# Optimization experiments

Hardware: AMD Instinct MI355X
Metric: run time of the kernel (lower is better)

Reference implementation:

```python
import jax, jax.numpy as jnp
import numpy as np

B, GL, GF, N = 4, 4, 128, 1024
CS, CN, NA = 32, 16, 16
S, HS = 512, 512


def squash(s, axis):
    # mag_sq/(1+mag_sq) * s/mag == s * mag/(1+mag_sq)
    mag_sq = jnp.sum(s * s, axis=axis, keepdims=True)
    return s * (jnp.sqrt(mag_sq) / (1.0 + mag_sq))


def routing(u_hat, n_iter=3):
    # u_hat: [M, I, J, U]; dynamic routing, softmax over J, squash over J (as in source)
    M, I, J, U = u_hat.shape
    b = jnp.zeros((I, J), dtype=u_hat.dtype)
    v = None
    for _ in range(n_iter):
        c = jax.nn.softmax(b, axis=1)                       # [I, J]
        s = jnp.einsum('ij,miju->mju', c, u_hat)            # [M, J, U]
        v = squash(s, axis=1)                               # squash over J (torch dim=2)
        b = b + jnp.einsum('miju,mju->mij', u_hat, v).mean(axis=0)
    return v


def setup_inputs():
    key = jax.random.key(0)
    ks = jax.random.split(key, 7)
    sc = 0.1
    return {
        'graph_embed': jax.random.normal(ks[0], (B, GL, GF, N), jnp.float32),
        'hidden': jax.random.normal(ks[1], (B, S, HS), jnp.float32),
        'Wp': jax.random.normal(ks[2], (GL, CS, GL, GF), jnp.float32) * sc,  # per-unit conv kernels
        'bp': jax.random.normal(ks[3], (GL, CS), jnp.float32) * sc,
        'Wg': jax.random.normal(ks[4], (CS, CN, CS, GL), jnp.float32) * sc,  # graph caps [I,J,U,K]
        'Wa': jax.random.normal(ks[5], (CS + HS,), jnp.float32) * sc,        # attention_1 weight
        'Ws': jax.random.normal(ks[6], (CN, NA, CS, CS), jnp.float32) * sc,  # aspect caps [I,J,U,K]
    }


def _per_example(x, h, Wp, bp, Wg, Wa, Ws):
    # x: [GL, GF, N], h: [S, HS]
    gl, gf, n = x.shape
    # primary capsules: each unit's conv kernel covers all (GL,GF) -> full contraction
    u = jnp.einsum('uclf,lfn->ucn', Wp, x) + bp[:, :, None]   # [GL, CS, N]
    u = squash(u.reshape(gl, -1), axis=1)                     # squash over CS*N (torch dim=2)
    p = u.reshape(n, gl, CS)                                  # torch .view(-1, GL, CS)
    # graph capsule routing
    u_hat_g = jnp.einsum('ijuk,mik->miju', Wg, p.transpose(0, 2, 1))  # [N, CS, CN, CS]
    v_g = routing(u_hat_g)                                    # [N, CN, CS]
    g = v_g.reshape(n, CS, CN).mean(axis=0).reshape(CN, CS)   # torch .view semantics
    # adaptive attention: Linear([g;h]) with no bias, softmax over capsules
    score = jax.nn.softmax((g @ Wa[:CS])[None, :] + (h @ Wa[CS:])[:, None], axis=1)  # [S, CN]
    condensed = g[None, :, :] * score[:, :, None]             # [S, CN, CS]
    # aspect capsule routing (transpose(1,2) then layer-internal transpose cancel out)
    u_hat_a = jnp.einsum('ijuk,mik->miju', Ws, condensed)     # [S, CN, NA, CS]
    return routing(u_hat_a)                                   # [S, NA, CS]


def reference(graph_embed, hidden, Wp, bp, Wg, Wa, Ws):
    f = jax.vmap(_per_example, in_axes=(0, 0, None, None, None, None, None))
    return f(graph_embed, hidden, Wp, bp, Wg, Wa, Ws)   # [B, S, NA, CS]
```

## Files before the change

### kernel.cpp

```cpp
#include <hip/hip_runtime.h>
#include <math.h>


static constexpr int OFF_U   = 0;
static constexpr int OFF_S   = 524288;
static constexpr int OFF_SSP = 2621440;
static constexpr int OFF_BGP = 2621696;
static constexpr int OFF_GP  = 2654464;
static constexpr int OFF_VA  = 2687232;
static constexpr int OFF_MS  = 2689280;
static constexpr int OFF_UH  = 2820352;
static constexpr int OFF_WGR = 2853120;

__global__ void k_primaryF(const float* __restrict__ X, const float* __restrict__ Wp,
                           const float* __restrict__ bp,
                           float* __restrict__ U, float* __restrict__ SSp,
                           const float* __restrict__ Wg, float* __restrict__ Wgr)
{
    __shared__ float Wt[128 * 68];
    __shared__ float red[256];
    const int t = threadIdx.x;
    if (blockIdx.z == 4) {
        const int blk = blockIdx.x * 16 + blockIdx.y;
#pragma unroll
        for (int r = 0; r < 8; ++r) {
            const int e = blk * 2048 + r * 256 + t;
            const int q = e >> 9, rem = e & 511;
            const int u = rem >> 4, j = rem & 15;
            const int i = q & 31, kk = q >> 5;
            Wgr[e] = Wg[((i * 16 + j) * 32 + u) * 4 + kk];
        }
        return;
    }
    const int ct = blockIdx.x, nt = blockIdx.y, b = blockIdx.z;
    const int tn = t & 15, tc = t >> 4;
    const int c0 = ct * 64, n0 = nt * 64;
    float acc[4][4] = {};
    for (int ks = 0; ks < 4; ++ks) {
        if (ks) __syncthreads();
#pragma unroll
        for (int i = 0; i < 8; ++i) {
            const int idx = t + i * 256;
            const int c = idx >> 5, k4 = idx & 31;
            const float4 wv = *(const float4*)&Wp[(size_t)(c0 + c) * 512 + ks * 128 + k4 * 4];
            Wt[(k4 * 4 + 0) * 68 + c] = wv.x;
            Wt[(k4 * 4 + 1) * 68 + c] = wv.y;
            Wt[(k4 * 4 + 2) * 68 + c] = wv.z;
            Wt[(k4 * 4 + 3) * 68 + c] = wv.w;
        }
        __syncthreads();
        const float* Xp = X + (size_t)b * 524288 + (size_t)(ks * 128) * 1024 + n0 + tn * 4;
#pragma unroll 4
        for (int k = 0; k < 128; ++k) {
            const float4 xv = *(const float4*)(Xp + (size_t)k * 1024);
            const float4 wv = *(const float4*)&Wt[k * 68 + tc * 4];
            const float w[4] = {wv.x, wv.y, wv.z, wv.w};
            const float x[4] = {xv.x, xv.y, xv.z, xv.w};
#pragma unroll
            for (int ci = 0; ci < 4; ++ci)
#pragma unroll
                for (int ni = 0; ni < 4; ++ni)
                    acc[ci][ni] = fmaf(w[ci], x[ni], acc[ci][ni]);
        }
    }
    float ssq = 0.f;
#pragma unroll
    for (int ci = 0; ci < 4; ++ci) {
        const int c = c0 + tc * 4 + ci;
        const float bv = bp[c];
        float4 o = make_float4(acc[ci][0] + bv, acc[ci][1] + bv,
                               acc[ci][2] + bv, acc[ci][3] + bv);
        ssq = fmaf(o.x, o.x, ssq); ssq = fmaf(o.y, o.y, ssq);
        ssq = fmaf(o.z, o.z, ssq); ssq = fmaf(o.w, o.w, ssq);
        *(float4*)&U[(size_t)b * 131072 + (size_t)c * 1024 + n0 + tn * 4] = o;
    }
    red[t] = ssq;
    __syncthreads();
    for (int s = 64; s > 0; s >>= 1) {
        if ((t & 127) < s) red[t] += red[t + s];
        __syncthreads();
    }
    if ((t & 127) == 0)
        SSp[(b * 4 + ct * 2 + (t >> 7)) * 16 + nt] = red[t];
}

__global__ __launch_bounds__(256) void k_smatmulM2(
    const float* __restrict__ U, const float* __restrict__ SSp,
    const float* __restrict__ Bgp, const float* __restrict__ Wgr,
    float* __restrict__ S, float* __restrict__ MS, float* __restrict__ Gp,
    const int bg0)
{
    __shared__ __align__(16) float Pt[64 * 68];
    __shared__ __align__(16) float Ct[64 * 160];
    __shared__ float cls[512];
    __shared__ float bgs[512];
    __shared__ float gacc[128];
    const int mt = blockIdx.x, us = blockIdx.y, b = blockIdx.z;
    const int t = threadIdx.x;
    const int tm = t >> 4;
    const int uu = t & 7, jh = (t >> 3) & 1;
    const int m0 = mt * 64;

    if (bg0) {
        cls[t] = 0.0625f;
        cls[t + 256] = 0.0625f;
    } else {
#pragma unroll
        for (int h = 0; h < 2; ++h) {
            const int p = t + h * 256;
            const int i = p >> 4, j = p & 15;
            float s = 0.f;
#pragma unroll 4
            for (int mc = 0; mc < 16; ++mc)
                s += Bgp[((b * 16 + mc) * 8 + (j >> 1)) * 64 + i * 2 + (j & 1)];
            bgs[p] = s * (1.f / 1024.f);
        }
        __syncthreads();
        if (t < 32) {
            float vals[16];
            float mx = -1e30f;
            for (int j = 0; j < 16; ++j) { vals[j] = bgs[t * 16 + j]; mx = fmaxf(mx, vals[j]); }
            float sum = 0.f;
            for (int j = 0; j < 16; ++j) { vals[j] = expf(vals[j] - mx); sum += vals[j]; }
            const float inv = 1.f / sum;
            for (int j = 0; j < 16; ++j) cls[t * 16 + j] = vals[j] * inv;
        }
    }
    if (Gp != nullptr && t < 128) gacc[t] = 0.f;
    float ssum = 0.f;
#pragma unroll
    for (int i = 0; i < 16; ++i) ssum += SSp[(b * 4 + (mt >> 2)) * 16 + i];
    const float sc = sqrtf(ssum) / (1.f + ssum);
    float acc[4][8] = {};
    const float* Ub = U + (size_t)b * 131072 + (size_t)m0 * 128;
    __syncthreads();

    for (int kc = 0; kc < 2; ++kc) {
#pragma unroll
        for (int it = 0; it < 4; ++it) {
            const int x = t + it * 256;
            const int m = x & 63, q4 = x >> 6;
            const float4 v = *(const float4*)&Ub[(size_t)m * 128 + kc * 64 + q4 * 4];
            Pt[(q4 * 4 + 0) * 68 + m] = v.x * sc;
            Pt[(q4 * 4 + 1) * 68 + m] = v.y * sc;
            Pt[(q4 * 4 + 2) * 68 + m] = v.z * sc;
            Pt[(q4 * 4 + 3) * 68 + m] = v.w * sc;
        }
#pragma unroll
        for (int it = 0; it < 8; ++it) {
            const int x = t + it * 256;
            const int c4 = (x & 31) * 4, qL = x >> 5;
            const int q = kc * 64 + qL;
            const int i = q & 31;
            const int j0 = c4 & 15;
            const float4 w = *(const float4*)&Wgr[(size_t)q * 512 + us * 128 + c4];
            const int cp = qL * 160 + c4 + ((c4 >> 4) << 2);
            Ct[cp + 0] = cls[i * 16 + j0 + 0] * w.x;
            Ct[cp + 1] = cls[i * 16 + j0 + 1] * w.y;
            Ct[cp + 2] = cls[i * 16 + j0 + 2] * w.z;
            Ct[cp + 3] = cls[i * 16 + j0 + 3] * w.w;
        }
        __syncthreads();
        const int cbase = uu * 20 + jh * 8;
#pragma unroll 4
        for (int qL = 0; qL < 64; ++qL) {
            const float4 p4 = *(const float4*)&Pt[qL * 68 + tm * 4];
            const float4 ca = *(const float4*)&Ct[qL * 160 + cbase];
            const float4 cb = *(const float4*)&Ct[qL * 160 + cbase + 4];
            const float pm[4] = {p4.x, p4.y, p4.z, p4.w};
            const float cj[8] = {ca.x, ca.y, ca.z, ca.w, cb.x, cb.y, cb.z, cb.w};
#pragma unroll
            for (int mm = 0; mm < 4; ++mm)
#pragma unroll
                for (int jj = 0; jj < 8; ++jj)
                    acc[mm][jj] = fmaf(pm[mm], cj[jj], acc[mm][jj]);
        }
        __syncthreads();
    }

#pragma unroll
    for (int mm = 0; mm < 4; ++mm) {
        float* Sp = S + (size_t)b * 524288 + (size_t)(m0 + tm * 4 + mm) * 512 + us * 8 + uu;
#pragma unroll
        for (int jj = 0; jj < 8; ++jj)
            Sp[(jh * 8 + jj) * 32] = acc[mm][jj];
    }

    if (Gp == nullptr) {
#pragma unroll
        for (int mm = 0; mm < 4; ++mm) {
            float msq = 0.f;
#pragma unroll
            for (int jj = 0; jj < 8; ++jj) msq = fmaf(acc[mm][jj], acc[mm][jj], msq);
            msq += __shfl_xor(msq, 8);
            if (jh == 0)
                MS[b * 32768 + (m0 + tm * 4 + mm) * 32 + us * 8 + uu] =
                    sqrtf(msq) / (1.f + msq);
        }
    } else {
        float part[8];
#pragma unroll
        for (int jj = 0; jj < 8; ++jj) part[jj] = 0.f;
#pragma unroll
        for (int mm = 0; mm < 4; ++mm) {
            float msq = 0.f;
#pragma unroll
            for (int jj = 0; jj < 8; ++jj) msq = fmaf(acc[mm][jj], acc[mm][jj], msq);
            msq += __shfl_xor(msq, 8);
            const float msc = sqrtf(msq) / (1.f + msq);
#pragma unroll
            for (int jj = 0; jj < 8; ++jj) part[jj] = fmaf(acc[mm][jj], msc, part[jj]);
        }
#pragma unroll
        for (int jj = 0; jj < 8; ++jj)
            atomicAdd(&gacc[(jh * 8 + jj) * 8 + uu], part[jj]);
        __syncthreads();
        if (t < 128) {
            const int j = t >> 3, u2 = t & 7;
            Gp[(size_t)(b * 16 + mt) * 512 + j * 32 + us * 8 + u2] =
                gacc[t] * (1.f / 1024.f);
        }
    }
}

__global__ void k_tbu2(const float* __restrict__ U, const float* __restrict__ SSp,
                       const float* __restrict__ S, const float* __restrict__ MS,
                       const float* __restrict__ Wg, float* __restrict__ Bgp,
                       const int first)
{
    __shared__ float Ps[64 * 132];
    __shared__ float Vs[64 * 68];
    __shared__ float bup[64];
    const int jt = blockIdx.x, mc = blockIdx.y, b = blockIdx.z;
    const int t = threadIdx.x;
    const int tq = t & 31, tjv = t >> 5;
    const int m0 = mc * 64;
    if (t < 64) bup[t] = 0.f;
    float ssum = 0.f;
#pragma unroll
    for (int i = 0; i < 16; ++i) ssum += SSp[(b * 4 + (mc >> 2)) * 16 + i];
    const float sc = sqrtf(ssum) / (1.f + ssum);
#pragma unroll
    for (int i = 0; i < 8; ++i) {
        const int f4 = t + i * 256;
        const int r = f4 >> 5, q4 = f4 & 31;
        float4 v = *(const float4*)&U[(size_t)b * 131072 + (size_t)(m0 + r) * 128 + q4 * 4];
        v.x *= sc; v.y *= sc; v.z *= sc; v.w *= sc;
        *(float4*)&Ps[r * 132 + q4 * 4] = v;
    }
#pragma unroll
    for (int i = 0; i < 4; ++i) {
        const int f4 = t + i * 256;
        const int r = f4 >> 4, c4 = f4 & 15;
        const int m = m0 + r;
        float4 v = *(const float4*)&S[(size_t)b * 524288 + (size_t)m * 512 + jt * 64 + c4 * 4];
        const int ub = (c4 * 4) & 31;
        const float* msp = MS + b * 32768 + m * 32;
        v.x *= msp[ub + 0]; v.y *= msp[ub + 1]; v.z *= msp[ub + 2]; v.w *= msp[ub + 3];
        *(float4*)&Vs[r * 68 + c4 * 4] = v;
    }
    __syncthreads();
    float acc[4][8] = {};
#pragma unroll 2
    for (int m = 0; m < 64; ++m) {
        const float4 p4 = *(const float4*)&Ps[m * 132 + tq * 4];
        const float4 va = *(const float4*)&Vs[m * 68 + tjv * 8];
        const float4 vb = *(const float4*)&Vs[m * 68 + tjv * 8 + 4];
        const float pv[4] = {p4.x, p4.y, p4.z, p4.w};
        const float vv[8] = {va.x, va.y, va.z, va.w, vb.x, vb.y, vb.z, vb.w};
#pragma unroll
        for (int qi = 0; qi < 4; ++qi)
#pragma unroll
            for (int ji = 0; ji < 8; ++ji)
                acc[qi][ji] = fmaf(pv[qi], vv[ji], acc[qi][ji]);
    }
    const int k = tq >> 3;
    const int j_loc = tjv >> 2;
    const int j = jt * 2 + j_loc;
    const int u0 = (tjv & 3) * 8;
#pragma unroll
    for (int qi = 0; qi < 4; ++qi) {
        const int i = (tq & 7) * 4 + qi;
        const float* wp = Wg + ((i * 16 + j) * 32) * 4 + k;
        float s = 0.f;
#pragma unroll
        for (int ji = 0; ji < 8; ++ji)
            s = fmaf(wp[(u0 + ji) * 4], acc[qi][ji], s);
        s += __shfl_xor(s, 8);
        s += __shfl_xor(s, 16);
        s += __shfl_xor(s, 32);
        if ((t & 56) == 0) atomicAdd(&bup[i * 2 + j_loc], s);
    }
    __syncthreads();
    if (t < 64) {
        float* slot = &Bgp[((b * 16 + mc) * 8 + jt) * 64 + t];
        if (first) *slot = bup[t];
        else       *slot += bup[t];
    }
}

__global__ void k_uhat2(const float* __restrict__ Gp, const float* __restrict__ Wa,
                        const float* __restrict__ Ws, float* __restrict__ UH)
{
    const int b = blockIdx.y;
    const int t = threadIdx.x;
    __shared__ float g[512], cond[512], score[16], red[16];
    float g0 = 0.f, g1 = 0.f;
#pragma unroll 4
    for (int mt = 0; mt < 16; ++mt) {
        const float* gp = Gp + (size_t)(b * 16 + mt) * 512;
        g0 += gp[t];
        g1 += gp[t + 256];
    }
    g[t] = g0;
    g[t + 256] = g1;
    __syncthreads();
    if (t < 16) {
        float s = 0.f;
        for (int u = 0; u < 32; ++u) s = fmaf(g[t * 32 + u], Wa[u], s);
        red[t] = s;
    }
    __syncthreads();
    if (t == 0) {
        float mx = -1e30f;
        for (int j = 0; j < 16; ++j) mx = fmaxf(mx, red[j]);
        float sum = 0.f;
        for (int j = 0; j < 16; ++j) { score[j] = expf(red[j] - mx); sum += score[j]; }
        const float inv = 1.f / sum;
        for (int j = 0; j < 16; ++j) score[j] *= inv;
    }
    __syncthreads();
    cond[t] = g[t] * score[t >> 5];
    cond[t + 256] = g[t + 256] * score[(t + 256) >> 5];
    __syncthreads();
    const int e0 = blockIdx.x * 1024 + t * 4;
    const int i = e0 >> 9;
    const float* cp = cond + i * 32;
    const float* wp = Ws + (size_t)e0 * 32;
    float res[4];
#pragma unroll
    for (int jj = 0; jj < 4; ++jj) {
        float s = 0.f;
#pragma unroll
        for (int k8 = 0; k8 < 8; ++k8) {
            const float4 w = *(const float4*)(wp + jj * 32 + k8 * 4);
            s = fmaf(w.x, cp[k8 * 4 + 0], s);
            s = fmaf(w.y, cp[k8 * 4 + 1], s);
            s = fmaf(w.z, cp[k8 * 4 + 2], s);
            s = fmaf(w.w, cp[k8 * 4 + 3], s);
        }
        res[jj] = s;
    }
    ((float4*)UH)[(b * 8192 + e0) >> 2] = make_float4(res[0], res[1], res[2], res[3]);
}

__global__ void k_route(const float* __restrict__ UH, float* __restrict__ VA)
{
    const int b = blockIdx.x;
    const int t = threadIdx.x;
    __shared__ float uh[8192], ba[256], cc[256], sbuf[512], msc[32];
#pragma unroll
    for (int i = 0; i < 8; ++i)
        ((float4*)uh)[i * 256 + t] = ((const float4*)UH)[b * 2048 + i * 256 + t];
    ba[t] = 0.f;
    __syncthreads();
    for (int it = 0; it < 3; ++it) {
        if (t < 16) {
            float mx = -1e30f;
            for (int j = 0; j < 16; ++j) mx = fmaxf(mx, ba[t * 16 + j]);
            float sum = 0.f;
            for (int j = 0; j < 16; ++j) { cc[t * 16 + j] = expf(ba[t * 16 + j] - mx); sum += cc[t * 16 + j]; }
            const float inv = 1.f / sum;
            for (int j = 0; j < 16; ++j) cc[t * 16 + j] *= inv;
        }
        __syncthreads();
        for (int h = 0; h < 2; ++h) {
            const int e = h * 256 + t;
            const int j = e >> 5;
            float s = 0.f;
            for (int i = 0; i < 16; ++i) s = fmaf(cc[i * 16 + j], uh[i * 512 + e], s);
            sbuf[e] = s;
        }
        __syncthreads();
        if (t < 32) {
            float mg = 0.f;
            for (int j = 0; j < 16; ++j) { const float x = sbuf[j * 32 + t]; mg = fmaf(x, x, mg); }
            msc[t] = sqrtf(mg) / (1.f + mg);
        }
        __syncthreads();
        for (int h = 0; h < 2; ++h) {
            const int e = h * 256 + t;
            sbuf[e] *= msc[e & 31];
        }
        __syncthreads();
        if (it < 2) {
            const int i = t >> 4, j = t & 15;
            float s = 0.f;
            for (int u = 0; u < 32; ++u) s = fmaf(uh[i * 512 + j * 32 + u], sbuf[j * 32 + u], s);
            ba[t] += s;
            __syncthreads();
        }
    }
    VA[b * 512 + t] = sbuf[t];
    VA[b * 512 + 256 + t] = sbuf[256 + t];
}

__global__ void k_out(const float* __restrict__ VA, float* __restrict__ out)
{
    const int idx = blockIdx.x * 256 + threadIdx.x;
    const int b = idx >> 16;
    const int jv4 = idx & 127;
    ((float4*)out)[idx] = ((const float4*)VA)[b * 128 + jv4];
}

extern "C" void kernel_launch(void* const* d_in, const int* in_sizes, int n_in,
                              void* d_out, int out_size, void* d_ws, size_t ws_size,
                              hipStream_t stream)
{
    const float* X   = (const float*)d_in[0];
    const float* Wp  = (const float*)d_in[2];
    const float* bp  = (const float*)d_in[3];
    const float* Wg  = (const float*)d_in[4];
    const float* Wa  = (const float*)d_in[5];
    const float* Wsp = (const float*)d_in[6];
    float* out = (float*)d_out;
    float* ws = (float*)d_ws;

    float* U   = ws + OFF_U;
    float* S   = ws + OFF_S;
    float* SSp = ws + OFF_SSP;
    float* Bgp = ws + OFF_BGP;
    float* Gp  = ws + OFF_GP;
    float* VA  = ws + OFF_VA;
    float* MS  = ws + OFF_MS;
    float* UH  = ws + OFF_UH;
    float* Wgr = ws + OFF_WGR;


    k_primaryF<<<dim3(2, 16, 5), 256, 0, stream>>>(X, Wp, bp, U, SSp, Wg, Wgr);

    k_smatmulM2<<<dim3(16, 4, 4), 256, 0, stream>>>(U, SSp, Bgp, Wgr, S, MS, nullptr, 1);
    k_tbu2<<<dim3(8, 16, 4), 256, 0, stream>>>(U, SSp, S, MS, Wg, Bgp, 1);
    k_smatmulM2<<<dim3(16, 4, 4), 256, 0, stream>>>(U, SSp, Bgp, Wgr, S, MS, nullptr, 0);
    k_tbu2<<<dim3(8, 16, 4), 256, 0, stream>>>(U, SSp, S, MS, Wg, Bgp, 0);
    k_smatmulM2<<<dim3(16, 4, 4), 256, 0, stream>>>(U, SSp, Bgp, Wgr, S, nullptr, Gp, 0);

    k_uhat2<<<dim3(8, 4), 256, 0, stream>>>(Gp, Wa, Wsp, UH);
    k_route<<<4, 256, 0, stream>>>(UH, VA);
    k_out<<<1024, 256, 0, stream>>>(VA, out);
}
```

Before: 230.6 us.

## Split primary capsule conv along K and reduce partials in separate kernel

```diff
diff --git a/kernel.cpp b/kernel.cpp
--- a/kernel.cpp
+++ b/kernel.cpp
@@ -12,15 +12,13 @@
 static constexpr int OFF_UH  = 2820352;
 static constexpr int OFF_WGR = 2853120;
 
-__global__ void k_primaryF(const float* __restrict__ X, const float* __restrict__ Wp,
-                           const float* __restrict__ bp,
-                           float* __restrict__ U, float* __restrict__ SSp,
-                           const float* __restrict__ Wg, float* __restrict__ Wgr)
+__global__ void k_primary_part(const float* __restrict__ X, const float* __restrict__ Wp,
+                               float* __restrict__ Upart,
+                               const float* __restrict__ Wg, float* __restrict__ Wgr)
 {
     __shared__ float Wt[128 * 68];
-    __shared__ float red[256];
     const int t = threadIdx.x;
-    if (blockIdx.z == 4) {
+    if (blockIdx.z == 16) {
         const int blk = blockIdx.x * 16 + blockIdx.y;
 #pragma unroll
         for (int r = 0; r < 8; ++r) {
@@ -32,56 +30,72 @@
         }
         return;
     }
-    const int ct = blockIdx.x, nt = blockIdx.y, b = blockIdx.z;
+    const int ct = blockIdx.x, nt = blockIdx.y;
+    const int b = blockIdx.z >> 2, ks = blockIdx.z & 3;
     const int tn = t & 15, tc = t >> 4;
     const int c0 = ct * 64, n0 = nt * 64;
+#pragma unroll
+    for (int i = 0; i < 8; ++i) {
+        const int idx = t + i * 256;
+        const int c = idx >> 5, k4 = idx & 31;
+        const float4 wv = *(const float4*)&Wp[(size_t)(c0 + c) * 512 + ks * 128 + k4 * 4];
+        Wt[(k4 * 4 + 0) * 68 + c] = wv.x;
+        Wt[(k4 * 4 + 1) * 68 + c] = wv.y;
+        Wt[(k4 * 4 + 2) * 68 + c] = wv.z;
+        Wt[(k4 * 4 + 3) * 68 + c] = wv.w;
+    }
+    __syncthreads();
     float acc[4][4] = {};
-    for (int ks = 0; ks < 4; ++ks) {
-        if (ks) __syncthreads();
-#pragma unroll
-        for (int i = 0; i < 8; ++i) {
-            const int idx = t + i * 256;
-            const int c = idx >> 5, k4 = idx & 31;
-            const float4 wv = *(const float4*)&Wp[(size_t)(c0 + c) * 512 + ks * 128 + k4 * 4];
-            Wt[(k4 * 4 + 0) * 68 + c] = wv.x;
-            Wt[(k4 * 4 + 1) * 68 + c] = wv.y;
-            Wt[(k4 * 4 + 2) * 68 + c] = wv.z;
-            Wt[(k4 * 4 + 3) * 68 + c] = wv.w;
-        }
-        __syncthreads();
-        const float* Xp = X + (size_t)b * 524288 + (size_t)(ks * 128) * 1024 + n0 + tn * 4;
+    const float* Xp = X + (size_t)b * 524288 + (size_t)(ks * 128) * 1024 + n0 + tn * 4;
 #pragma unroll 4
-        for (int k = 0; k < 128; ++k) {
-            const float4 xv = *(const float4*)(Xp + (size_t)k * 1024);
-            const float4 wv = *(const float4*)&Wt[k * 68 + tc * 4];
-            const float w[4] = {wv.x, wv.y, wv.z, wv.w};
-            const float x[4] = {xv.x, xv.y, xv.z, xv.w};
-#pragma unroll
-            for (int ci = 0; ci < 4; ++ci)
-#pragma unroll
-                for (int ni = 0; ni < 4; ++ni)
-                    acc[ci][ni] = fmaf(w[ci], x[ni], acc[ci][ni]);
-        }
-    }
+    for (int k = 0; k < 128; ++k) {
+        const float4 xv = *(const float4*)(Xp + (size_t)k * 1024);
+        const float4 wv = *(const float4*)&Wt[k * 68 + tc * 4];
+        const float w[4] = {wv.x, wv.y, wv.z, wv.w};
+        const float x[4] = {xv.x, xv.y, xv.z, xv.w};
+#pragma unroll
+        for (int ci = 0; ci < 4; ++ci)
+#pragma unroll
+            for (int ni = 0; ni < 4; ++ni)
+                acc[ci][ni] = fmaf(w[ci], x[ni], acc[ci][ni]);
+    }
+    float* up = Upart + (size_t)ks * 524288 + (size_t)b * 131072;
+#pragma unroll
+    for (int ci = 0; ci < 4; ++ci)
+        *(float4*)&up[(size_t)(c0 + tc * 4 + ci) * 1024 + n0 + tn * 4] =
+            make_float4(acc[ci][0], acc[ci][1], acc[ci][2], acc[ci][3]);
+}
+
+__global__ void k_reduceU(const float* __restrict__ Upart, const float* __restrict__ bp,
+                          float* __restrict__ U, float* __restrict__ SSp)
+{
+    __shared__ float red[256];
+    const int blk = blockIdx.x, t = threadIdx.x;
+    const int b = blk >> 5, cg = blk & 31;
     float ssq = 0.f;
 #pragma unroll
-    for (int ci = 0; ci < 4; ++ci) {
-        const int c = c0 + tc * 4 + ci;
+    for (int i = 0; i < 4; ++i) {
+        const int c = cg * 4 + i;
+        const int f4 = b * 32768 + c * 256 + t;
+        float4 s = ((const float4*)Upart)[f4];
+#pragma unroll
+        for (int ks = 1; ks < 4; ++ks) {
+            const float4 p = ((const float4*)Upart)[ks * 131072 + f4];
+            s.x += p.x; s.y += p.y; s.z += p.z; s.w += p.w;
+        }
         const float bv = bp[c];
-        float4 o = make_float4(acc[ci][0] + bv, acc[ci][1] + bv,
-                               acc[ci][2] + bv, acc[ci][3] + bv);
-        ssq = fmaf(o.x, o.x, ssq); ssq = fmaf(o.y, o.y, ssq);
-        ssq = fmaf(o.z, o.z, ssq); ssq = fmaf(o.w, o.w, ssq);
-        *(float4*)&U[(size_t)b * 131072 + (size_t)c * 1024 + n0 + tn * 4] = o;
+        s.x += bv; s.y += bv; s.z += bv; s.w += bv;
+        ssq = fmaf(s.x, s.x, ssq); ssq = fmaf(s.y, s.y, ssq);
+        ssq = fmaf(s.z, s.z, ssq); ssq = fmaf(s.w, s.w, ssq);
+        ((float4*)U)[f4] = s;
     }
     red[t] = ssq;
     __syncthreads();
-    for (int s = 64; s > 0; s >>= 1) {
-        if ((t & 127) < s) red[t] += red[t + s];
-        __syncthreads();
-    }
-    if ((t & 127) == 0)
-        SSp[(b * 4 + ct * 2 + (t >> 7)) * 16 + nt] = red[t];
+    for (int s = 128; s > 0; s >>= 1) {
+        if (t < s) red[t] += red[t + s];
+        __syncthreads();
+    }
+    if (t == 0) SSp[(b * 4 + (cg >> 3)) * 8 + (cg & 7)] = red[0];
 }
 
 __global__ __launch_bounds__(256) void k_smatmulM2(
@@ -129,7 +143,7 @@
     if (Gp != nullptr && t < 128) gacc[t] = 0.f;
     float ssum = 0.f;
 #pragma unroll
-    for (int i = 0; i < 16; ++i) ssum += SSp[(b * 4 + (mt >> 2)) * 16 + i];
+    for (int i = 0; i < 8; ++i) ssum += SSp[(b * 4 + (mt >> 2)) * 8 + i];
     const float sc = sqrtf(ssum) / (1.f + ssum);
     float acc[4][8] = {};
     const float* Ub = U + (size_t)b * 131072 + (size_t)m0 * 128;
@@ -238,7 +252,7 @@
     if (t < 64) bup[t] = 0.f;
     float ssum = 0.f;
 #pragma unroll
-    for (int i = 0; i < 16; ++i) ssum += SSp[(b * 4 + (mc >> 2)) * 16 + i];
+    for (int i = 0; i < 8; ++i) ssum += SSp[(b * 4 + (mc >> 2)) * 8 + i];
     const float sc = sqrtf(ssum) / (1.f + ssum);
 #pragma unroll
     for (int i = 0; i < 8; ++i) {
@@ -437,7 +451,8 @@
     float* Wgr = ws + OFF_WGR;
 
 
-    k_primaryF<<<dim3(2, 16, 5), 256, 0, stream>>>(X, Wp, bp, U, SSp, Wg, Wgr);
+    k_primary_part<<<dim3(2, 16, 17), 256, 0, stream>>>(X, Wp, S, Wg, Wgr);
+    k_reduceU<<<128, 256, 0, stream>>>(S, bp, U, SSp);
 
     k_smatmulM2<<<dim3(16, 4, 4), 256, 0, stream>>>(U, SSp, Bgp, Wgr, S, MS, nullptr, 1);
     k_tbu2<<<dim3(8, 16, 4), 256, 0, stream>>>(U, SSp, S, MS, Wg, Bgp, 1);
```

Measured after the change: 196.3 us. -14.9%, faster.
